# Kernel tuning notes

Measured on AMD Instinct MI355X. Metric: run time of the kernel, lower is better.

The kernel has to match this reference:

```python
import jax, jax.numpy as jnp
import numpy as np

D_MODEL = 1024
N_HEADS = 16
HEAD_DIM = D_MODEL // N_HEADS


def setup_inputs() -> dict:
    key = jax.random.key(0)
    ks = jax.random.split(key, 9)
    B, T, S, D = 4, 2048, 512, D_MODEL
    sc = 1.0 / np.sqrt(D)
    return {
        "x": jax.random.normal(ks[0], (B, T, D), dtype=jnp.float32),
        "context": jax.random.normal(ks[1], (B, S, D), dtype=jnp.float32),
        "context_mask": jnp.ones((B, S), dtype=bool),
        "Wq": jax.random.normal(ks[2], (D, D), dtype=jnp.float32) * sc,
        "bq": jnp.zeros((D,), dtype=jnp.float32),
        "Wkv": jax.random.normal(ks[3], (D, 2 * D), dtype=jnp.float32) * sc,
        "bkv": jnp.zeros((2 * D,), dtype=jnp.float32),
        "Wp": jax.random.normal(ks[4], (D, D), dtype=jnp.float32) * sc,
        "bp": jnp.zeros((D,), dtype=jnp.float32),
    }


def reference(x, context, context_mask, Wq, bq, Wkv, bkv, Wp, bp):
    B, T, D = x.shape
    S = context.shape[1]
    H, Hd = N_HEADS, HEAD_DIM
    # projections
    q = (x @ Wq + bq).reshape(B, T, H, Hd).transpose(0, 2, 1, 3)          # [B,H,T,Hd]
    kv = (context @ Wkv + bkv).reshape(B, S, 2, H, Hd)
    k = kv[:, :, 0].transpose(0, 2, 1, 3)                                  # [B,H,S,Hd]
    v = kv[:, :, 1].transpose(0, 2, 1, 3)                                  # [B,H,S,Hd]
    # scaled dot-product attention with context mask
    scores = jnp.einsum("bhtd,bhsd->bhts", q, k) / np.sqrt(Hd)            # [B,H,T,S]
    neg_inf = jnp.finfo(scores.dtype).min
    scores = jnp.where(context_mask[:, None, None, :], scores, neg_inf)
    attn = jax.nn.softmax(scores, axis=-1)
    # dropout is identity in eval mode (p applied only in training)
    out = jnp.einsum("bhts,bhsd->bthd", attn, v).reshape(B, T, D)
    return out @ Wp + bp
```

## Files before the change

### kernel.cpp

```cpp
#include <hip/hip_runtime.h>

typedef __bf16 bf16x8 __attribute__((ext_vector_type(8)));
typedef float  f32x4  __attribute__((ext_vector_type(4)));

#define MFMA(a, b, c) __builtin_amdgcn_mfma_f32_16x16x32_bf16((a), (b), (c), 0, 0, 0)

#define GLL(g, l) __builtin_amdgcn_global_load_lds(                                  \
    (const __attribute__((address_space(1))) void*)(g),                              \
    (__attribute__((address_space(3))) void*)(l), 16, 0, 0)

#define BB 4
#define TT 2048
#define SS 512
#define DM 1024
#define NH 16
#define HD 64

__device__ __forceinline__ unsigned short f2bh(float f) {
    __bf16 h = (__bf16)f;
    union { __bf16 h; unsigned short u; } v; v.h = h;
    return v.u;
}

__device__ __forceinline__ void tcast_tile(const float* __restrict__ in,
                                           unsigned short* __restrict__ out,
                                           int K, int N, int n0, int k0,
                                           float (*tile)[33], int tid) {
    int tx = tid & 31, ty = tid >> 5;
#pragma unroll
    for (int r = 0; r < 32; r += 8)
        tile[ty + r][tx] = in[(k0 + ty + r) * N + n0 + tx];
    __syncthreads();
    int r2 = tid >> 3, cg = (tid & 7) * 4;
    ushort4 o;
    o.x = f2bh(tile[cg + 0][r2]);
    o.y = f2bh(tile[cg + 1][r2]);
    o.z = f2bh(tile[cg + 2][r2]);
    o.w = f2bh(tile[cg + 3][r2]);
    *(ushort4*)&out[(n0 + r2) * K + k0 + cg] = o;
}

__global__ __launch_bounds__(256)
void prep(const float4* __restrict__ x, const float4* __restrict__ ctx,
          const unsigned int* __restrict__ mw,
          const float* __restrict__ Wq, const float* __restrict__ Wkv,
          const float* __restrict__ Wp,
          ushort4* __restrict__ Xbf, ushort4* __restrict__ Cbf,
          unsigned short* __restrict__ WqT, unsigned short* __restrict__ WkvT,
          unsigned short* __restrict__ WpT, float* __restrict__ mbias) {
    __shared__ float tile[32][33];
    __shared__ int flags[2];
    const int bid = blockIdx.x, tid = threadIdx.x;
    if (bid < 8192) {
        int i = bid * 256 + tid;
        float4 v = x[i];
        ushort4 o; o.x = f2bh(v.x); o.y = f2bh(v.y); o.z = f2bh(v.z); o.w = f2bh(v.w);
        Xbf[i] = o;
    } else if (bid < 10240) {
        int i = (bid - 8192) * 256 + tid;
        float4 v = ctx[i];
        ushort4 o; o.x = f2bh(v.x); o.y = f2bh(v.y); o.z = f2bh(v.z); o.w = f2bh(v.w);
        Cbf[i] = o;
    } else if (bid < 11264) {
        int loc = bid - 10240;
        tcast_tile(Wq, WqT, DM, DM, (loc & 31) * 32, (loc >> 5) * 32, tile, tid);
    } else if (bid < 13312) {
        int loc = bid - 11264;
        tcast_tile(Wkv, WkvT, DM, 2 * DM, (loc & 63) * 32, (loc >> 6) * 32, tile, tid);
    } else if (bid < 14336) {
        int loc = bid - 13312;
        tcast_tile(Wp, WpT, DM, DM, (loc & 31) * 32, (loc >> 5) * 32, tile, tid);
    } else {
        if (tid == 0) { flags[0] = 1; flags[1] = 1; }
        __syncthreads();
        int okI = 1, okF = 1;
        for (int i = tid; i < 512; i += 256) {
            unsigned int w = mw[i];
            if (w > 1u) okI = 0;
            if (w != 0u && w != 0x3f800000u) okF = 0;
        }
        if (!okI) atomicAnd(&flags[0], 0);
        if (!okF) atomicAnd(&flags[1], 0);
        __syncthreads();
        bool wordLayout = (flags[0] != 0) || (flags[1] != 0);
        const unsigned char* mb = (const unsigned char*)mw;
        for (int s = tid; s < BB * SS; s += 256) {
            bool on = wordLayout ? (mw[s] != 0u) : (mb[s] != 0);
            mbias[s] = on ? 0.0f : -1e38f;
        }
    }
}

__device__ __forceinline__ void gemm_core(
    const unsigned short* __restrict__ A, const unsigned short* __restrict__ Bt,
    int K, int m0, int n0, unsigned short* As, unsigned short* Bs,
    f32x4 (*acc)[4]) {
    const int tid = threadIdx.x;
    const int w = tid >> 6, l = tid & 63;
    const int quad = l >> 4, col = l & 15;
    const int wm = w * 64;
    const int arow = tid >> 3;
    const int apiece = (tid & 7) ^ (arow & 7);
    const unsigned short* Ab = A + (size_t)(m0 + arow) * K + apiece * 8;
    const unsigned short* Bb = Bt + (size_t)(n0 + arow) * K + apiece * 8;

    for (int k0 = 0; k0 < K; k0 += 64) {
        __syncthreads();
#pragma unroll
        for (int g = 0; g < 8; ++g)
            GLL(Ab + k0 + g * 16 * K, &As[g * 1024 + tid * 8]);
#pragma unroll
        for (int g = 0; g < 4; ++g)
            GLL(Bb + k0 + g * 16 * K, &Bs[g * 1024 + tid * 8]);
        __syncthreads();
#pragma unroll
        for (int k32 = 0; k32 < 2; ++k32) {
            bf16x8 af[4], bf[4];
#pragma unroll
            for (int i = 0; i < 4; i++) {
                int rr = wm + i * 16 + col;
                af[i] = *(const bf16x8*)&As[rr * 64 + (((k32 * 4 + quad) ^ (rr & 7)) * 8)];
            }
#pragma unroll
            for (int j = 0; j < 4; j++) {
                int rr = j * 16 + col;
                bf[j] = *(const bf16x8*)&Bs[rr * 64 + (((k32 * 4 + quad) ^ (rr & 7)) * 8)];
            }
#pragma unroll
            for (int i = 0; i < 4; i++)
#pragma unroll
                for (int j = 0; j < 4; j++) acc[i][j] = MFMA(af[i], bf[j], acc[i][j]);
        }
    }
}

__global__ __launch_bounds__(128, 3)
void gemm_qkv(const unsigned short* __restrict__ Xbf, const unsigned short* __restrict__ WqT,
              const float* __restrict__ bq, unsigned short* __restrict__ Qb,
              const unsigned short* __restrict__ Cbf, const unsigned short* __restrict__ WkvT,
              const float* __restrict__ bkv, unsigned short* __restrict__ Kb,
              unsigned short* __restrict__ Vtb) {
    __shared__ __align__(16) unsigned short As[128 * 64];
    __shared__ __align__(16) unsigned short Bs[64 * 64];
    const int tid = threadIdx.x;
    const int w = tid >> 6, l = tid & 63;
    const int quad = l >> 4, col = l & 15;
    const int bid = blockIdx.x;

    const f32x4 zero = {0.f, 0.f, 0.f, 0.f};
    f32x4 acc[4][4];
#pragma unroll
    for (int i = 0; i < 4; i++)
#pragma unroll
        for (int j = 0; j < 4; j++) acc[i][j] = zero;

    if (bid < 1024) {
        const int xg = bid & 7, t = bid >> 3;
        const int m0 = (xg + 8 * (t & 7)) * 128;
        const int n0 = (t >> 3) * 64;
        gemm_core(Xbf, WqT, DM, m0, n0, As, Bs, acc);
        const float QS = 0.125f * 1.4426950408889634f;
#pragma unroll
        for (int i = 0; i < 4; i++) {
#pragma unroll
            for (int j = 0; j < 4; j++) {
                int n = n0 + j * 16 + col;
                int mb = m0 + w * 64 + i * 16 + quad * 4;
                float bv = bq[n];
#pragma unroll
                for (int ii = 0; ii < 4; ii++)
                    Qb[(mb + ii) * DM + n] = f2bh((acc[i][j][ii] + bv) * QS);
            }
        }
    } else {
        const int loc = bid - 1024;
        const int xg = loc & 7, t = loc >> 3;
        const int m0 = (xg + 8 * (t & 1)) * 128;
        const int n0 = (t >> 1) * 64;
        gemm_core(Cbf, WkvT, DM, m0, n0, As, Bs, acc);
#pragma unroll
        for (int i = 0; i < 4; i++) {
#pragma unroll
            for (int j = 0; j < 4; j++) {
                int n = n0 + j * 16 + col;
                int mb = m0 + w * 64 + i * 16 + quad * 4;
                float bv = bkv[n];
                if (n < 1024) {
                    int h = n >> 6, d = n & 63;
#pragma unroll
                    for (int ii = 0; ii < 4; ii++) {
                        int m = mb + ii; int b = m >> 9, s = m & 511;
                        Kb[(((b * NH + h) * SS) + s) * HD + d] = f2bh(acc[i][j][ii] + bv);
                    }
                } else {
                    int q = n - 1024; int h = q >> 6, d = q & 63;
#pragma unroll
                    for (int ii = 0; ii < 4; ii++) {
                        int m = mb + ii; int b = m >> 9, s = m & 511;
                        Vtb[(((b * NH + h) * HD) + d) * SS + s] = f2bh(acc[i][j][ii] + bv);
                    }
                }
            }
        }
    }
}

__global__ __launch_bounds__(128, 3)
void gemm_out(const unsigned short* __restrict__ Ob, const unsigned short* __restrict__ WpT,
              const float* __restrict__ bp, float* __restrict__ out) {
    __shared__ __align__(16) unsigned short As[128 * 64];
    __shared__ __align__(16) unsigned short Bs[64 * 64];
    const int tid = threadIdx.x;
    const int w = tid >> 6, l = tid & 63;
    const int quad = l >> 4, col = l & 15;
    const int bid = blockIdx.x;
    const int xg = bid & 7, t = bid >> 3;
    const int m0 = (xg + 8 * (t & 7)) * 128;
    const int n0 = (t >> 3) * 64;

    const f32x4 zero = {0.f, 0.f, 0.f, 0.f};
    f32x4 acc[4][4];
#pragma unroll
    for (int i = 0; i < 4; i++)
#pragma unroll
        for (int j = 0; j < 4; j++) acc[i][j] = zero;

    gemm_core(Ob, WpT, DM, m0, n0, As, Bs, acc);

#pragma unroll
    for (int i = 0; i < 4; i++) {
#pragma unroll
        for (int j = 0; j < 4; j++) {
            int n = n0 + j * 16 + col;
            int mb = m0 + w * 64 + i * 16 + quad * 4;
            float bv = bp[n];
#pragma unroll
            for (int ii = 0; ii < 4; ii++)
                out[(mb + ii) * DM + n] = acc[i][j][ii] + bv;
        }
    }
}

__global__ __launch_bounds__(512, 4)
void flash_attn(const unsigned short* __restrict__ Q, const unsigned short* __restrict__ Kb,
                const unsigned short* __restrict__ Vt, const float* __restrict__ mbias,
                unsigned short* __restrict__ O) {
    const int bid = blockIdx.x;
    const int xg = bid & 7, tq = bid >> 3;
    const int tb = tq & 7;
    const int bh = xg + 8 * (tq >> 3);
    const int b = bh >> 4;
    const int tid = threadIdx.x;
    const int w = tid >> 6, l = tid & 63;
    const int quad = l >> 4, col = l & 15;

    __shared__ __align__(16) unsigned short Ks[2][64 * 64];
    __shared__ __align__(16) unsigned short Vs[2][64 * 64];
    __shared__ __align__(16) unsigned short Pb[8][32 * 40];
    __shared__ float biasS[SS];

    const unsigned short* Kh = Kb + bh * SS * HD;
    const unsigned short* Vh = Vt + bh * HD * SS;

    biasS[tid] = mbias[b * SS + tid];

    const int rowbase = b * TT + tb * 256 + w * 32;
    bf16x8 qf[2][2];
#pragma unroll
    for (int rg = 0; rg < 2; rg++) {
        const unsigned short* qrow = Q + (rowbase + rg * 16 + col) * DM + (bh & 15) * HD;
        qf[rg][0] = *(const bf16x8*)(qrow + quad * 8);
        qf[rg][1] = *(const bf16x8*)(qrow + 32 + quad * 8);
    }

    const int sr = tid >> 3, sp = tid & 7;
    const int spk = ((sp ^ (sr & 7)) * 8);
    const int kgo = sr * HD + spk;
    const int vgo = sr * SS + spk;

    GLL(Kh + kgo, &Ks[0][tid * 8]);
    GLL(Vh + vgo, &Vs[0][tid * 8]);

    const f32x4 zero = {0.f, 0.f, 0.f, 0.f};
    f32x4 o[2][4];
#pragma unroll
    for (int rg = 0; rg < 2; rg++)
#pragma unroll
        for (int j = 0; j < 4; j++) o[rg][j] = zero;
    f32x4 lsum[2] = {zero, zero};

    for (int it = 0; it < SS / 64; ++it) {
        const int s0 = it * 64;
        const int buf = it & 1;
        __syncthreads();
        if (it + 1 < SS / 64) {
            GLL(Kh + (s0 + 64) * HD + kgo, &Ks[buf ^ 1][tid * 8]);
            GLL(Vh + (s0 + 64) + vgo, &Vs[buf ^ 1][tid * 8]);
        }

#pragma unroll
        for (int h2 = 0; h2 < 2; ++h2) {
            f32x4 sc[2][2];
#pragma unroll
            for (int jj = 0; jj < 2; ++jj) {
                int row = (2 * h2 + jj) * 16 + col;
                bf16x8 k0 = *(const bf16x8*)&Ks[buf][row * 64 + ((quad ^ (row & 7)) * 8)];
                bf16x8 k1 = *(const bf16x8*)&Ks[buf][row * 64 + (((4 + quad) ^ (row & 7)) * 8)];
#pragma unroll
                for (int rg = 0; rg < 2; rg++) {
                    f32x4 tt = MFMA(qf[rg][0], k0, zero);
                    sc[rg][jj] = MFMA(qf[rg][1], k1, tt);
                }
            }
#pragma unroll
            for (int rg = 0; rg < 2; rg++) {
#pragma unroll
                for (int jj = 0; jj < 2; jj++) {
                    float bb = biasS[s0 + (2 * h2 + jj) * 16 + col];
#pragma unroll
                    for (int i = 0; i < 4; i++) {
                        float p = exp2f(sc[rg][jj][i] + bb);
                        lsum[rg][i] += p;
                        Pb[w][(rg * 16 + quad * 4 + i) * 40 + jj * 16 + col] = f2bh(p);
                    }
                }
            }
            asm volatile("s_waitcnt lgkmcnt(0)" ::: "memory");
            bf16x8 pf[2];
#pragma unroll
            for (int rg = 0; rg < 2; rg++)
                pf[rg] = *(const bf16x8*)&Pb[w][(rg * 16 + col) * 40 + quad * 8];
#pragma unroll
            for (int j2 = 0; j2 < 4; j2++) {
                int row = j2 * 16 + col;
                bf16x8 vf = *(const bf16x8*)&Vs[buf][row * 64 + (((h2 * 4 + quad) ^ (row & 7)) * 8)];
#pragma unroll
                for (int rg = 0; rg < 2; rg++)
                    o[rg][j2] = MFMA(pf[rg], vf, o[rg][j2]);
            }
            asm volatile("" ::: "memory");
        }
    }

#pragma unroll
    for (int rg = 0; rg < 2; rg++) {
#pragma unroll
        for (int i = 0; i < 4; i++) {
            float rs = lsum[rg][i];
#pragma unroll
            for (int off = 1; off < 16; off <<= 1) rs += __shfl_xor(rs, off);
            float inv = 1.0f / rs;
            unsigned short* orow = O + (rowbase + rg * 16 + quad * 4 + i) * DM
                                     + (bh & 15) * HD + col;
#pragma unroll
            for (int j2 = 0; j2 < 4; j2++)
                orow[j2 * 16] = f2bh(o[rg][j2][i] * inv);
        }
    }
}

extern "C" void kernel_launch(void* const* d_in, const int* in_sizes, int n_in,
                              void* d_out, int out_size, void* d_ws, size_t ws_size,
                              hipStream_t stream) {
    const float* x    = (const float*)d_in[0];
    const float* ctx  = (const float*)d_in[1];
    const void*  cmsk = d_in[2];
    const float* Wq   = (const float*)d_in[3];
    const float* bq   = (const float*)d_in[4];
    const float* Wkv  = (const float*)d_in[5];
    const float* bkv  = (const float*)d_in[6];
    const float* Wp   = (const float*)d_in[7];
    const float* bp   = (const float*)d_in[8];
    float* out = (float*)d_out;

    char* ws = (char*)d_ws;
    size_t off = 0;
    auto alloc = [&](size_t bytes) -> void* {
        void* p = ws + off;
        off += (bytes + 255) & ~(size_t)255;
        return p;
    };
    const size_t NX = (size_t)BB * TT * DM;
    const size_t NC = (size_t)BB * SS * DM;
    unsigned short* Xbf  = (unsigned short*)alloc(NX * 2);
    unsigned short* Cbf  = (unsigned short*)alloc(NC * 2);
    unsigned short* WqT  = (unsigned short*)alloc((size_t)DM * DM * 2);
    unsigned short* WkvT = (unsigned short*)alloc((size_t)DM * 2 * DM * 2);
    unsigned short* WpT  = (unsigned short*)alloc((size_t)DM * DM * 2);
    unsigned short* Qb   = (unsigned short*)alloc(NX * 2);
    unsigned short* Kbf  = (unsigned short*)alloc(NC * 2);
    unsigned short* Vtb  = (unsigned short*)alloc(NC * 2);
    unsigned short* Ob   = (unsigned short*)alloc(NX * 2);
    float* mbias         = (float*)alloc((size_t)BB * SS * 4);

    prep<<<14337, 256, 0, stream>>>((const float4*)x, (const float4*)ctx,
                                    (const unsigned int*)cmsk, Wq, Wkv, Wp,
                                    (ushort4*)Xbf, (ushort4*)Cbf,
                                    WqT, WkvT, WpT, mbias);

    gemm_qkv<<<1536, 128, 0, stream>>>(Xbf, WqT, bq, Qb, Cbf, WkvT, bkv, Kbf, Vtb);

    flash_attn<<<BB * NH * (TT / 256), 512, 0, stream>>>(Qb, Kbf, Vtb, mbias, Ob);

    gemm_out<<<1024, 128, 0, stream>>>(Ob, WpT, bp, out);
}
```

Measured before the change: 202.6 us.

## Enlarge GEMM tiles to 128x128 and compute softmax row sums with MFMA

```diff
diff --git a/kernel.cpp b/kernel.cpp
--- a/kernel.cpp
+++ b/kernel.cpp
@@ -96,9 +96,10 @@
     int K, int m0, int n0, unsigned short* As, unsigned short* Bs,
     f32x4 (*acc)[4]) {
     const int tid = threadIdx.x;
-    const int w = tid >> 6, l = tid & 63;
+    const int l = tid & 63;
     const int quad = l >> 4, col = l & 15;
-    const int wm = w * 64;
+    const int w = tid >> 6;
+    const int wm = (w & 1) * 64, wn = (w >> 1) * 64;
     const int arow = tid >> 3;
     const int apiece = (tid & 7) ^ (arow & 7);
     const unsigned short* Ab = A + (size_t)(m0 + arow) * K + apiece * 8;
@@ -107,15 +108,15 @@
     for (int k0 = 0; k0 < K; k0 += 64) {
         __syncthreads();
 #pragma unroll
-        for (int g = 0; g < 8; ++g)
-            GLL(Ab + k0 + g * 16 * K, &As[g * 1024 + tid * 8]);
-#pragma unroll
         for (int g = 0; g < 4; ++g)
-            GLL(Bb + k0 + g * 16 * K, &Bs[g * 1024 + tid * 8]);
+            GLL(Ab + k0 + g * 32 * K, &As[g * 2048 + tid * 8]);
+#pragma unroll
+        for (int g = 0; g < 4; ++g)
+            GLL(Bb + k0 + g * 32 * K, &Bs[g * 2048 + tid * 8]);
         __syncthreads();
 #pragma unroll
         for (int k32 = 0; k32 < 2; ++k32) {
-            bf16x8 af[4], bf[4];
+            bf16x8 af[4], bfr[4];
 #pragma unroll
             for (int i = 0; i < 4; i++) {
                 int rr = wm + i * 16 + col;
@@ -123,28 +124,30 @@
             }
 #pragma unroll
             for (int j = 0; j < 4; j++) {
-                int rr = j * 16 + col;
-                bf[j] = *(const bf16x8*)&Bs[rr * 64 + (((k32 * 4 + quad) ^ (rr & 7)) * 8)];
+                int rr = wn + j * 16 + col;
+                bfr[j] = *(const bf16x8*)&Bs[rr * 64 + (((k32 * 4 + quad) ^ (rr & 7)) * 8)];
             }
 #pragma unroll
             for (int i = 0; i < 4; i++)
 #pragma unroll
-                for (int j = 0; j < 4; j++) acc[i][j] = MFMA(af[i], bf[j], acc[i][j]);
-        }
-    }
-}
-
-__global__ __launch_bounds__(128, 3)
+                for (int j = 0; j < 4; j++) acc[i][j] = MFMA(af[i], bfr[j], acc[i][j]);
+        }
+    }
+}
+
+__global__ __launch_bounds__(256, 3)
 void gemm_qkv(const unsigned short* __restrict__ Xbf, const unsigned short* __restrict__ WqT,
               const float* __restrict__ bq, unsigned short* __restrict__ Qb,
               const unsigned short* __restrict__ Cbf, const unsigned short* __restrict__ WkvT,
               const float* __restrict__ bkv, unsigned short* __restrict__ Kb,
               unsigned short* __restrict__ Vtb) {
     __shared__ __align__(16) unsigned short As[128 * 64];
-    __shared__ __align__(16) unsigned short Bs[64 * 64];
+    __shared__ __align__(16) unsigned short Bs[128 * 64];
     const int tid = threadIdx.x;
-    const int w = tid >> 6, l = tid & 63;
+    const int l = tid & 63;
     const int quad = l >> 4, col = l & 15;
+    const int w = tid >> 6;
+    const int wm = (w & 1) * 64, wn = (w >> 1) * 64;
     const int bid = blockIdx.x;
 
     const f32x4 zero = {0.f, 0.f, 0.f, 0.f};
@@ -154,18 +157,18 @@
 #pragma unroll
         for (int j = 0; j < 4; j++) acc[i][j] = zero;
 
-    if (bid < 1024) {
+    if (bid < 512) {
         const int xg = bid & 7, t = bid >> 3;
         const int m0 = (xg + 8 * (t & 7)) * 128;
-        const int n0 = (t >> 3) * 64;
+        const int n0 = (t >> 3) * 128;
         gemm_core(Xbf, WqT, DM, m0, n0, As, Bs, acc);
         const float QS = 0.125f * 1.4426950408889634f;
 #pragma unroll
         for (int i = 0; i < 4; i++) {
 #pragma unroll
             for (int j = 0; j < 4; j++) {
-                int n = n0 + j * 16 + col;
-                int mb = m0 + w * 64 + i * 16 + quad * 4;
+                int n = n0 + wn + j * 16 + col;
+                int mb = m0 + wm + i * 16 + quad * 4;
                 float bv = bq[n];
 #pragma unroll
                 for (int ii = 0; ii < 4; ii++)
@@ -173,17 +176,17 @@
             }
         }
     } else {
-        const int loc = bid - 1024;
+        const int loc = bid - 512;
         const int xg = loc & 7, t = loc >> 3;
         const int m0 = (xg + 8 * (t & 1)) * 128;
-        const int n0 = (t >> 1) * 64;
+        const int n0 = (t >> 1) * 128;
         gemm_core(Cbf, WkvT, DM, m0, n0, As, Bs, acc);
 #pragma unroll
         for (int i = 0; i < 4; i++) {
 #pragma unroll
             for (int j = 0; j < 4; j++) {
-                int n = n0 + j * 16 + col;
-                int mb = m0 + w * 64 + i * 16 + quad * 4;
+                int n = n0 + wn + j * 16 + col;
+                int mb = m0 + wm + i * 16 + quad * 4;
                 float bv = bkv[n];
                 if (n < 1024) {
                     int h = n >> 6, d = n & 63;
@@ -205,18 +208,20 @@
     }
 }
 
-__global__ __launch_bounds__(128, 3)
+__global__ __launch_bounds__(256, 3)
 void gemm_out(const unsigned short* __restrict__ Ob, const unsigned short* __restrict__ WpT,
               const float* __restrict__ bp, float* __restrict__ out) {
     __shared__ __align__(16) unsigned short As[128 * 64];
-    __shared__ __align__(16) unsigned short Bs[64 * 64];
+    __shared__ __align__(16) unsigned short Bs[128 * 64];
     const int tid = threadIdx.x;
-    const int w = tid >> 6, l = tid & 63;
+    const int l = tid & 63;
     const int quad = l >> 4, col = l & 15;
+    const int w = tid >> 6;
+    const int wm = (w & 1) * 64, wn = (w >> 1) * 64;
     const int bid = blockIdx.x;
     const int xg = bid & 7, t = bid >> 3;
     const int m0 = (xg + 8 * (t & 7)) * 128;
-    const int n0 = (t >> 3) * 64;
+    const int n0 = (t >> 3) * 128;
 
     const f32x4 zero = {0.f, 0.f, 0.f, 0.f};
     f32x4 acc[4][4];
@@ -231,8 +236,8 @@
     for (int i = 0; i < 4; i++) {
 #pragma unroll
         for (int j = 0; j < 4; j++) {
-            int n = n0 + j * 16 + col;
-            int mb = m0 + w * 64 + i * 16 + quad * 4;
+            int n = n0 + wn + j * 16 + col;
+            int mb = m0 + wm + i * 16 + quad * 4;
             float bv = bp[n];
 #pragma unroll
             for (int ii = 0; ii < 4; ii++)
@@ -256,13 +261,15 @@
 
     __shared__ __align__(16) unsigned short Ks[2][64 * 64];
     __shared__ __align__(16) unsigned short Vs[2][64 * 64];
-    __shared__ __align__(16) unsigned short Pb[8][32 * 40];
+    __shared__ __align__(16) unsigned short Pb[8][2][32 * 32];
     __shared__ float biasS[SS];
 
     const unsigned short* Kh = Kb + bh * SS * HD;
     const unsigned short* Vh = Vt + bh * HD * SS;
 
-    biasS[tid] = mbias[b * SS + tid];
+    float bval = mbias[b * SS + tid];
+    biasS[tid] = bval;
+    const int allon = __syncthreads_and(bval == 0.0f);
 
     const int rowbase = b * TT + tb * 256 + w * 32;
     bf16x8 qf[2][2];
@@ -287,7 +294,10 @@
     for (int rg = 0; rg < 2; rg++)
 #pragma unroll
         for (int j = 0; j < 4; j++) o[rg][j] = zero;
-    f32x4 lsum[2] = {zero, zero};
+    f32x4 lacc[2] = {zero, zero};
+    bf16x8 onesb;
+#pragma unroll
+    for (int z = 0; z < 8; z++) onesb[z] = (__bf16)1.0f;
 
     for (int it = 0; it < SS / 64; ++it) {
         const int s0 = it * 64;
@@ -306,30 +316,57 @@
                 int row = (2 * h2 + jj) * 16 + col;
                 bf16x8 k0 = *(const bf16x8*)&Ks[buf][row * 64 + ((quad ^ (row & 7)) * 8)];
                 bf16x8 k1 = *(const bf16x8*)&Ks[buf][row * 64 + (((4 + quad) ^ (row & 7)) * 8)];
+                __builtin_amdgcn_s_setprio(1);
 #pragma unroll
                 for (int rg = 0; rg < 2; rg++) {
                     f32x4 tt = MFMA(qf[rg][0], k0, zero);
                     sc[rg][jj] = MFMA(qf[rg][1], k1, tt);
                 }
-            }
+                __builtin_amdgcn_s_setprio(0);
+            }
+            if (allon) {
+#pragma unroll
+                for (int rg = 0; rg < 2; rg++)
+#pragma unroll
+                    for (int jj = 0; jj < 2; jj++)
+#pragma unroll
+                        for (int i = 0; i < 4; i++) {
+                            float p = exp2f(sc[rg][jj][i]);
+                            int row = rg * 16 + quad * 4 + i;
+                            int s = jj * 16 + col;
+                            int pc = (s >> 3) ^ ((row >> 1) & 3);
+                            Pb[w][h2][(row << 5) + (pc << 3) + (s & 7)] = f2bh(p);
+                        }
+            } else {
+#pragma unroll
+                for (int rg = 0; rg < 2; rg++)
+#pragma unroll
+                    for (int jj = 0; jj < 2; jj++) {
+                        float bb = biasS[s0 + (2 * h2 + jj) * 16 + col];
+#pragma unroll
+                        for (int i = 0; i < 4; i++) {
+                            float p = exp2f(sc[rg][jj][i] + bb);
+                            int row = rg * 16 + quad * 4 + i;
+                            int s = jj * 16 + col;
+                            int pc = (s >> 3) ^ ((row >> 1) & 3);
+                            Pb[w][h2][(row << 5) + (pc << 3) + (s & 7)] = f2bh(p);
+                        }
+                    }
+            }
+        }
+
+#pragma unroll
+        for (int h2 = 0; h2 < 2; ++h2) {
+            bf16x8 pf[2];
 #pragma unroll
             for (int rg = 0; rg < 2; rg++) {
-#pragma unroll
-                for (int jj = 0; jj < 2; jj++) {
-                    float bb = biasS[s0 + (2 * h2 + jj) * 16 + col];
-#pragma unroll
-                    for (int i = 0; i < 4; i++) {
-                        float p = exp2f(sc[rg][jj][i] + bb);
-                        lsum[rg][i] += p;
-                        Pb[w][(rg * 16 + quad * 4 + i) * 40 + jj * 16 + col] = f2bh(p);
-                    }
-                }
-            }
-            asm volatile("s_waitcnt lgkmcnt(0)" ::: "memory");
-            bf16x8 pf[2];
-#pragma unroll
-            for (int rg = 0; rg < 2; rg++)
-                pf[rg] = *(const bf16x8*)&Pb[w][(rg * 16 + col) * 40 + quad * 8];
+                int prow = rg * 16 + col;
+                int pp = quad ^ ((col >> 1) & 3);
+                pf[rg] = *(const bf16x8*)&Pb[w][h2][(prow << 5) + (pp << 3)];
+            }
+            __builtin_amdgcn_s_setprio(1);
+#pragma unroll
+            for (int rg = 0; rg < 2; rg++) lacc[rg] = MFMA(pf[rg], onesb, lacc[rg]);
 #pragma unroll
             for (int j2 = 0; j2 < 4; j2++) {
                 int row = j2 * 16 + col;
@@ -338,7 +375,7 @@
                 for (int rg = 0; rg < 2; rg++)
                     o[rg][j2] = MFMA(pf[rg], vf, o[rg][j2]);
             }
-            asm volatile("" ::: "memory");
+            __builtin_amdgcn_s_setprio(0);
         }
     }
 
@@ -346,10 +383,7 @@
     for (int rg = 0; rg < 2; rg++) {
 #pragma unroll
         for (int i = 0; i < 4; i++) {
-            float rs = lsum[rg][i];
-#pragma unroll
-            for (int off = 1; off < 16; off <<= 1) rs += __shfl_xor(rs, off);
-            float inv = 1.0f / rs;
+            float inv = 1.0f / lacc[rg][i];
             unsigned short* orow = O + (rowbase + rg * 16 + quad * 4 + i) * DM
                                      + (bh & 15) * HD + col;
 #pragma unroll
@@ -398,9 +432,9 @@
                                     (ushort4*)Xbf, (ushort4*)Cbf,
                                     WqT, WkvT, WpT, mbias);
 
-    gemm_qkv<<<1536, 128, 0, stream>>>(Xbf, WqT, bq, Qb, Cbf, WkvT, bkv, Kbf, Vtb);
+    gemm_qkv<<<768, 256, 0, stream>>>(Xbf, WqT, bq, Qb, Cbf, WkvT, bkv, Kbf, Vtb);
 
     flash_attn<<<BB * NH * (TT / 256), 512, 0, stream>>>(Qb, Kbf, Vtb, mbias, Ob);
 
-    gemm_out<<<1024, 128, 0, stream>>>(Ob, WpT, bp, out);
-}
+    gemm_out<<<512, 256, 0, stream>>>(Ob, WpT, bp, out);
+}
```

Result: slower. 208.9 us (+3.1%).
